# Kernel tuning notes

Hardware: AMD Instinct MI355X
Metric: run time of the kernel (lower is better)

## Reference

```python
import jax, jax.numpy as jnp
import numpy as np

B, S, HID = 16, 577, 768
H, D = 12, 64          # heads, head_dim
N_KEEP = 576           # kept channels after structured pruning


def setup_inputs() -> dict:
    key = jax.random.key(0)
    ks = jax.random.split(key, 10)
    hs = jax.random.normal(ks[0], (B, S, HID), dtype=jnp.float32)
    Wq = jax.random.normal(ks[1], (HID, N_KEEP), dtype=jnp.float32) * 0.02
    bq = jax.random.normal(ks[2], (N_KEEP,), dtype=jnp.float32) * 0.02
    Wk = jax.random.normal(ks[3], (HID, N_KEEP), dtype=jnp.float32) * 0.02
    bk = jax.random.normal(ks[4], (N_KEEP,), dtype=jnp.float32) * 0.02
    Wv = jax.random.normal(ks[5], (HID, N_KEEP), dtype=jnp.float32) * 0.02
    bv = jax.random.normal(ks[6], (N_KEEP,), dtype=jnp.float32) * 0.02
    # positions of nonzero entries of the boolean padding masks (unique, sorted)
    q_idx = jnp.sort(jax.random.permutation(ks[7], HID)[:N_KEEP]).astype(jnp.int32)
    k_idx = jnp.sort(jax.random.permutation(ks[8], HID)[:N_KEEP]).astype(jnp.int32)
    v_idx = jnp.sort(jax.random.permutation(ks[9], HID)[:N_KEEP]).astype(jnp.int32)
    return {"hidden_states": hs, "Wq": Wq, "bq": bq, "Wk": Wk, "bk": bk,
            "Wv": Wv, "bv": bv, "q_idx": q_idx, "k_idx": k_idx, "v_idx": v_idx}


def _pad_and_split_heads(x, idx):
    # scatter pruned channels [B,S,N_KEEP] back into full layout [B,S,HID],
    # then split into heads -> [B,H,S,D]
    padded = jnp.zeros((B, S, HID), dtype=x.dtype).at[:, :, idx].set(x)
    return padded.reshape(B, S, H, D).transpose(0, 2, 1, 3)


def reference(hidden_states, Wq, bq, Wk, bk, Wv, bv, q_idx, k_idx, v_idx):
    q = hidden_states @ Wq + bq            # [B,S,N_KEEP]
    k = hidden_states @ Wk + bk
    v = hidden_states @ Wv + bv
    ql = _pad_and_split_heads(q, q_idx)     # [B,H,S,D]
    kl = _pad_and_split_heads(k, k_idx)
    vl = _pad_and_split_heads(v, v_idx)
    scale = 1.0 / np.float32(np.sqrt(D))
    scores = jnp.einsum('bhqd,bhkd->bhqk', ql, kl) * scale  # [B,H,S,S]
    probs = jax.nn.softmax(scores, axis=-1)
    ctx = jnp.einsum('bhqk,bhkd->bhqd', probs, vl)          # [B,H,S,D]
    ctx = ctx.transpose(0, 2, 1, 3).reshape(B, S, HID)       # [B,S,HID]
    return ctx[:, :, v_idx]                                  # gather kept channels
```

## Files before the change

### kernel.cpp

```cpp
#include <hip/hip_runtime.h>
#include <hip/hip_bf16.h>
#include <cstdint>
#include <cstddef>

#define B_     16
#define S_     577
#define SP_    584
#define HID_   768
#define H_     12
#define D_     64
#define NKEEP_ 576
#define MP_    (B_ * SP_)
#define NP4    (MP_ * HID_ / 4)

typedef __bf16 bf16;
typedef __bf16 bf16x8 __attribute__((ext_vector_type(8)));
typedef float  f32x4  __attribute__((ext_vector_type(4)));

__device__ __forceinline__ void gload16(const bf16* g, bf16* l) {
    __builtin_amdgcn_global_load_lds(
        (const __attribute__((address_space(1))) unsigned int*)g,
        (__attribute__((address_space(3))) unsigned int*)l, 16, 0, 0);
}

__device__ __forceinline__ float fexp2(float x) {
#if __has_builtin(__builtin_amdgcn_exp2f)
    return __builtin_amdgcn_exp2f(x);
#else
    return exp2f(x);
#endif
}

#define WAITBAR(N) asm volatile("s_waitcnt vmcnt(" #N ") lgkmcnt(0)\n\ts_barrier" ::: "memory")

__global__ __launch_bounds__(256) void k_prep(const float* __restrict__ hs,
                                              const float* __restrict__ Wq,
                                              const float* __restrict__ Wk,
                                              const float* __restrict__ Wv,
                                              const float* __restrict__ bq,
                                              const float* __restrict__ bk,
                                              const float* __restrict__ bv,
                                              const int* __restrict__ qi,
                                              const int* __restrict__ ki,
                                              const int* __restrict__ vi,
                                              bf16* __restrict__ hs_bf,
                                              bf16* __restrict__ Wp_t,
                                              int* __restrict__ inv,
                                              float* __restrict__ bias_p) {
    __shared__ float tile[64][33];
    const int bid = blockIdx.x, t = threadIdx.x;
    if (bid < 54) {
        const int p = bid / 18;
        const int j0 = (bid % 18) * 32;
        const float* W  = (p == 0) ? Wq : (p == 1) ? Wk : Wv;
        const int* idx  = (p == 0) ? qi : (p == 1) ? ki : vi;
        bf16* dst = Wp_t + (size_t)p * HID_ * HID_;
        const int lj = t & 31, lk = t >> 5;
        const int sj = t >> 3, ke = (t & 7) * 8;
        const int c = idx[j0 + sj];
        for (int kt = 0; kt < HID_; kt += 64) {
            __syncthreads();
#pragma unroll
            for (int i = 0; i < 8; ++i)
                tile[lk + i * 8][lj] = W[(size_t)(kt + lk + i * 8) * NKEEP_ + j0 + lj];
            __syncthreads();
            union { bf16 h[8]; bf16x8 v; } o;
#pragma unroll
            for (int i = 0; i < 8; ++i) o.h[i] = (bf16)tile[ke + i][sj];
            *reinterpret_cast<bf16x8*>(dst + (size_t)c * HID_ + kt + ke) = o.v;
        }
    } else if (bid == 54) {
        for (int i = t; i < 3 * HID_; i += 256) { inv[i] = -1; bias_p[i] = 0.0f; }
        __syncthreads();
        for (int i = t; i < 3 * NKEEP_; i += 256) {
            const int p = i / NKEEP_, j = i % NKEEP_;
            const int* src = (p == 0) ? qi : (p == 1) ? ki : vi;
            const float* bb = (p == 0) ? bq : (p == 1) ? bk : bv;
            const int c = src[j];
            inv[p * HID_ + c] = j;
            bias_p[p * HID_ + c] = bb[j];
        }
    } else {
        const int i = (bid - 55) * 256 + t;
        if (i < NP4) {
            const int row = i / 192;
            const int col = i - row * 192;
            const int b = row / SP_;
            const int s = row - b * SP_;
            uint2 ov = {0u, 0u};
            if (s < S_) {
                float4 v = reinterpret_cast<const float4*>(hs)[((size_t)(b * S_ + s)) * 192 + col];
                union { bf16 h[4]; uint2 u; } o;
                o.h[0] = (bf16)v.x; o.h[1] = (bf16)v.y;
                o.h[2] = (bf16)v.z; o.h[3] = (bf16)v.w;
                ov = o.u;
            }
            reinterpret_cast<uint2*>(hs_bf)[(size_t)row * 192 + col] = ov;
        }
    }
}

#define BM 128
#define BN 256
#define BK 32
#define BUFE 12288

__global__ __launch_bounds__(256, 2) void k_gemm(const bf16* __restrict__ X,
                                                 const bf16* __restrict__ Wp_t,
                                                 const float* __restrict__ bias_p,
                                                 bf16* __restrict__ Qo, bf16* __restrict__ Ko,
                                                 bf16* __restrict__ Vt) {
    __shared__ bf16 smem[3 * BUFE];

    const int xcd = blockIdx.x & 7, pos = blockIdx.x >> 3;
    const int L = xcd * 82 + (xcd > 0 ? 1 : 0) + pos;
    const int m0 = (L / 9) * BM;
    const int np = L % 9;
    const int n0 = (np % 3) * BN;
    const int p  = np / 3;

    const bf16* Wbase = Wp_t + (size_t)p * HID_ * HID_;
    const float osc = (p == 0) ? 0.125f * 1.44269504f : 1.0f;

    const int t = threadIdx.x;
    const int wid = t >> 6, lane = t & 63;
    const int wr = wid >> 1, wc = wid & 1;
    const int lrow = lane & 15, g = lane >> 4, lk = (lane >> 4) * 8;
    const int srow = lane >> 2, scol = (lane & 3) * 8;

    const bf16* Xs = X + (size_t)m0 * HID_;
    const bf16* Ws = Wbase + (size_t)n0 * HID_;

    f32x4 acc[4][8] = {};

#define STAGE(buf, kk)                                                          \
    {                                                                           \
        _Pragma("unroll")                                                       \
        for (int i_ = 0; i_ < 2; ++i_) {                                        \
            const int c_ = wid * 2 + i_;                                        \
            gload16(Xs + (size_t)(c_ * 16 + srow) * HID_ + (kk) + scol,         \
                    smem + (buf) * BUFE + c_ * 512);                            \
        }                                                                       \
        _Pragma("unroll")                                                       \
        for (int i_ = 0; i_ < 4; ++i_) {                                        \
            const int c_ = wid * 4 + i_;                                        \
            gload16(Ws + (size_t)(c_ * 16 + srow) * HID_ + (kk) + scol,         \
                    smem + (buf) * BUFE + 4096 + c_ * 512);                     \
        }                                                                       \
    }

#define COMPUTE(buf)                                                            \
    {                                                                           \
        const bf16* As_ = smem + (buf) * BUFE;                                  \
        const bf16* Bs_ = As_ + 4096;                                           \
        bf16x8 af[4], bfr[8];                                                   \
        _Pragma("unroll")                                                       \
        for (int m = 0; m < 4; ++m)                                             \
            af[m] = *reinterpret_cast<const bf16x8*>(                           \
                &As_[(wr * 64 + m * 16 + lrow) * BK + lk]);                     \
        _Pragma("unroll")                                                       \
        for (int n = 0; n < 8; ++n)                                             \
            bfr[n] = *reinterpret_cast<const bf16x8*>(                          \
                &Bs_[(wc * 128 + n * 16 + lrow) * BK + lk]);                    \
        _Pragma("unroll")                                                       \
        for (int m = 0; m < 4; ++m)                                             \
            _Pragma("unroll")                                                   \
            for (int n = 0; n < 8; ++n)                                         \
                acc[m][n] = __builtin_amdgcn_mfma_f32_16x16x32_bf16(            \
                    af[m], bfr[n], acc[m][n], 0, 0, 0);                         \
    }

    STAGE(0, 0)
    STAGE(1, BK)
    WAITBAR(6);

    int kk_next = 2 * BK;
    for (int u = 0; u < 7; ++u) {
#pragma unroll
        for (int j = 0; j < 3; ++j) {
            STAGE((j + 2) % 3, kk_next)
            COMPUTE(j)
            WAITBAR(6);
            kk_next += BK;
        }
    }
    STAGE(2, 23 * BK)
    COMPUTE(0)
    WAITBAR(6);
    COMPUTE(1)
    WAITBAR(0);
    COMPUTE(2)
#undef STAGE
#undef COMPUTE

    float bias_n[8];
#pragma unroll
    for (int n = 0; n < 8; ++n)
        bias_n[n] = bias_p[p * HID_ + n0 + wc * 128 + n * 16 + lrow];

    const int rowl = t >> 2, cq = t & 3;
#pragma unroll
    for (int half = 0; half < 2; ++half) {
        __syncthreads();
        if (wr == half) {
#pragma unroll
            for (int n = 0; n < 8; ++n)
#pragma unroll
                for (int m = 0; m < 4; ++m)
#pragma unroll
                    for (int r = 0; r < 4; ++r)
                        smem[(m * 16 + g * 4 + r) * 260 + wc * 128 + n * 16 + lrow] =
                            (bf16)((acc[m][n][r] + bias_n[n]) * osc);
        }
        __syncthreads();
        const int grow0 = m0 + half * 64;
        if (p < 2) {
            bf16* Obase = (p == 0) ? Qo : Ko;
            const int grow = grow0 + rowl;
            const int b = grow / SP_, s = grow - b * SP_;
            const size_t rbase = ((size_t)(b * H_ + 0) * SP_) * D_;
#pragma unroll
            for (int i = 0; i < 4; ++i) {
                const int c0 = i * 64 + cq * 8;
                (void)rbase; (void)c0;
            }
#pragma unroll
            for (int i = 0; i < 8; ++i) {
                const int c0 = i * 32 + cq * 8;
                bf16x8 v = *reinterpret_cast<const bf16x8*>(&smem[rowl * 260 + c0]);
                const int c = n0 + c0, h = c >> 6, d = c & 63;
                *reinterpret_cast<bf16x8*>(
                    &Obase[(((size_t)(b * H_ + h) * SP_) + s) * D_ + d]) = v;
            }
        } else {
            const int crow = n0 + t;
            bf16* vrow = Vt + (size_t)crow * MP_;
#pragma unroll
            for (int rg = 0; rg < 8; ++rg) {
                union { bf16 h8[8]; bf16x8 v; } pk;
#pragma unroll
                for (int i = 0; i < 8; ++i)
                    pk.h8[i] = smem[(rg * 8 + i) * 260 + t];
                *reinterpret_cast<bf16x8*>(&vrow[grow0 + rg * 8]) = pk.v;
            }
        }
    }
}

#define KB2  64
#define VLD2 72
#define KVSZ (KB2 * VLD2)

__global__ __launch_bounds__(512, 4) void k_attn(const bf16* __restrict__ Q,
                                                 const bf16* __restrict__ K,
                                                 const bf16* __restrict__ Vt,
                                                 const int* __restrict__ inv,
                                                 float* __restrict__ out) {
    __shared__ bf16 Ksm[2][KVSZ];
    __shared__ bf16 Vsm[2][KVSZ];

    const int bid = blockIdx.x;
    const int bh = bid % (B_ * H_);
    const int q0 = (bid / (B_ * H_)) * 128;
    const int t = threadIdx.x, wid = t >> 6, lane = t & 63;
    const int lcol = lane & 15, g = lane >> 4;
    const int b = bh / H_, h = bh % H_;

    const bf16* Qb = Q + (size_t)bh * SP_ * D_;
    const bf16* Kb = K + (size_t)bh * SP_ * D_;

    const int qrow = q0 + wid * 16 + lcol;
    bf16x8 qf0 = *reinterpret_cast<const bf16x8*>(Qb + (size_t)qrow * D_ + g * 8);
    bf16x8 qf1 = *reinterpret_cast<const bf16x8*>(Qb + (size_t)qrow * D_ + 32 + g * 8);

    const int key_t = t >> 3;
    const int a_t = t & 7;
    const int ch_t = a_t * 8;
    const bf16* Vrow = Vt + (size_t)(h * D_ + key_t) * MP_ + (size_t)b * SP_;

    float lrun = 0.f;
    f32x4 oT[4] = {};

    bf16x8 kreg = *reinterpret_cast<const bf16x8*>(Kb + (size_t)key_t * D_ + ch_t);
    bf16x8 vreg = *reinterpret_cast<const bf16x8*>(Vrow + ch_t);

    int cur = 0;
    for (int k0 = 0; k0 < S_; k0 += KB2) {
        *reinterpret_cast<bf16x8*>(&Ksm[cur][key_t * VLD2 + ch_t]) = kreg;
        *reinterpret_cast<bf16x8*>(&Vsm[cur][key_t * VLD2 + ch_t]) = vreg;
        __syncthreads();

        if (k0 + KB2 < S_) {
            kreg = *reinterpret_cast<const bf16x8*>(Kb + (size_t)(k0 + KB2 + key_t) * D_ + ch_t);
            vreg = *reinterpret_cast<const bf16x8*>(Vrow + k0 + KB2 + ch_t);
        }

        f32x4 sv[4];
        __builtin_amdgcn_s_setprio(1);
#pragma unroll
        for (int ks = 0; ks < 4; ++ks) {
            const bf16* kr = &Ksm[cur][(ks * 16 + lcol) * VLD2];
            bf16x8 kf0 = *reinterpret_cast<const bf16x8*>(kr + g * 8);
            bf16x8 kf1 = *reinterpret_cast<const bf16x8*>(kr + 32 + g * 8);
            f32x4 z = {};
            z = __builtin_amdgcn_mfma_f32_16x16x32_bf16(kf0, qf0, z, 0, 0, 0);
            z = __builtin_amdgcn_mfma_f32_16x16x32_bf16(kf1, qf1, z, 0, 0, 0);
            sv[ks] = z;
        }
        __builtin_amdgcn_s_setprio(0);
        if (k0 + KB2 > S_) {
#pragma unroll
            for (int ks = 0; ks < 4; ++ks)
#pragma unroll
                for (int r = 0; r < 4; ++r)
                    if (k0 + ks * 16 + g * 4 + r >= S_) sv[ks][r] = -INFINITY;
        }

        union { bf16 h[16]; bf16x8 v[2]; } pu;
        float rs = 0.f;
#pragma unroll
        for (int ks = 0; ks < 4; ++ks)
#pragma unroll
            for (int r = 0; r < 4; ++r) {
                float pv = fexp2(sv[ks][r]);
                rs += pv;
                pu.h[ks * 4 + r] = (bf16)pv;
            }
        lrun += rs;

        __builtin_amdgcn_s_setprio(1);
#pragma unroll
        for (int kh = 0; kh < 2; ++kh) {
#pragma unroll
            for (int tt = 0; tt < 4; ++tt) {
                const int d = tt * 16 + lcol;
                const bf16* vr = &Vsm[cur][d * VLD2 + kh * 32 + 4 * g];
                union { uint2 u[2]; bf16x8 v8; } vf;
                vf.u[0] = *reinterpret_cast<const uint2*>(vr);
                vf.u[1] = *reinterpret_cast<const uint2*>(vr + 16);
                oT[tt] = __builtin_amdgcn_mfma_f32_16x16x32_bf16(vf.v8, pu.v[kh], oT[tt], 0, 0, 0);
            }
        }
        __builtin_amdgcn_s_setprio(0);
        cur ^= 1;
    }

    lrun += __shfl_xor(lrun, 16);
    lrun += __shfl_xor(lrun, 32);

    if (qrow < S_) {
        const int* invv = inv + 2 * HID_;
        float invl = 1.0f / lrun;
        float* orow = out + ((size_t)b * S_ + qrow) * NKEEP_;
#pragma unroll
        for (int tt = 0; tt < 4; ++tt)
#pragma unroll
            for (int r = 0; r < 4; ++r) {
                int d = tt * 16 + g * 4 + r;
                int j = invv[h * D_ + d];
                if (j >= 0) orow[j] = oT[tt][r] * invl;
            }
    }
}

extern "C" void kernel_launch(void* const* d_in, const int* in_sizes, int n_in,
                              void* d_out, int out_size, void* d_ws, size_t ws_size,
                              hipStream_t stream) {
    const float* hs = (const float*)d_in[0];
    const float* Wq = (const float*)d_in[1];
    const float* bq = (const float*)d_in[2];
    const float* Wk = (const float*)d_in[3];
    const float* bk = (const float*)d_in[4];
    const float* Wv = (const float*)d_in[5];
    const float* bv = (const float*)d_in[6];
    const int* qi = (const int*)d_in[7];
    const int* ki = (const int*)d_in[8];
    const int* vi = (const int*)d_in[9];
    float* out = (float*)d_out;

    char* ws = (char*)d_ws;
    size_t off = 0;
    const size_t PAD = 8192;
    bf16* hs_bf = (bf16*)(ws + off); off += (size_t)MP_ * HID_ * 2 + PAD;
    bf16* Wp_t  = (bf16*)(ws + off); off += (size_t)3 * HID_ * HID_ * 2;
    float* bias_p = (float*)(ws + off); off += 3 * HID_ * 4;
    int* inv = (int*)(ws + off); off += 3 * HID_ * 4;
    bf16* Qw = (bf16*)(ws + off); off += (size_t)B_ * H_ * SP_ * D_ * 2 + PAD;
    bf16* Kw = (bf16*)(ws + off); off += (size_t)B_ * H_ * SP_ * D_ * 2 + PAD;
    bf16* Vt = (bf16*)(ws + off); off += (size_t)HID_ * MP_ * 2 + PAD;

    hipMemsetAsync(Wp_t, 0, (size_t)3 * HID_ * HID_ * 2, stream);
    const int nprep = 55 + (NP4 + 255) / 256;
    k_prep<<<nprep, 256, 0, stream>>>(hs, Wq, Wk, Wv, bq, bk, bv, qi, ki, vi,
                                      hs_bf, Wp_t, inv, bias_p);
    k_gemm<<<657, 256, 0, stream>>>(hs_bf, Wp_t, bias_p, Qw, Kw, Vt);
    k_attn<<<5 * B_ * H_, 512, 0, stream>>>(Qw, Kw, Vt, inv, out);
}
```

Measured before the change: 109.6 us.

## Replace triple-buffered GEMM pipeline with single-buffer loop; peel attention tail block

The QKV projection GEMM drops its three-stage async global-to-LDS pipeline with fine-grained waitcnt barriers. In its place is a simple single-buffer loop that syncs before and after each K-slice load, which shrinks LDS to allow more residency. The attention kernel peels the final partial key block out of the main loop, so the steady-state iterations lose the bounds check and masking branches. The GEMM change gives up load/compute overlap and will likely expose memory latency.

```diff
diff --git a/kernel.cpp b/kernel.cpp
--- a/kernel.cpp
+++ b/kernel.cpp
@@ -30,8 +30,6 @@
     return exp2f(x);
 #endif
 }
-
-#define WAITBAR(N) asm volatile("s_waitcnt vmcnt(" #N ") lgkmcnt(0)\n\ts_barrier" ::: "memory")
 
 __global__ __launch_bounds__(256) void k_prep(const float* __restrict__ hs,
                                               const float* __restrict__ Wq,
@@ -103,14 +101,14 @@
 #define BM 128
 #define BN 256
 #define BK 32
-#define BUFE 12288
+#define SMEME 16640
 
 __global__ __launch_bounds__(256, 2) void k_gemm(const bf16* __restrict__ X,
                                                  const bf16* __restrict__ Wp_t,
                                                  const float* __restrict__ bias_p,
                                                  bf16* __restrict__ Qo, bf16* __restrict__ Ko,
                                                  bf16* __restrict__ Vt) {
-    __shared__ bf16 smem[3 * BUFE];
+    __shared__ bf16 smem[SMEME];
 
     const int xcd = blockIdx.x & 7, pos = blockIdx.x >> 3;
     const int L = xcd * 82 + (xcd > 0 ? 1 : 0) + pos;
@@ -133,65 +131,35 @@
 
     f32x4 acc[4][8] = {};
 
-#define STAGE(buf, kk)                                                          \
-    {                                                                           \
-        _Pragma("unroll")                                                       \
-        for (int i_ = 0; i_ < 2; ++i_) {                                        \
-            const int c_ = wid * 2 + i_;                                        \
-            gload16(Xs + (size_t)(c_ * 16 + srow) * HID_ + (kk) + scol,         \
-                    smem + (buf) * BUFE + c_ * 512);                            \
-        }                                                                       \
-        _Pragma("unroll")                                                       \
-        for (int i_ = 0; i_ < 4; ++i_) {                                        \
-            const int c_ = wid * 4 + i_;                                        \
-            gload16(Ws + (size_t)(c_ * 16 + srow) * HID_ + (kk) + scol,         \
-                    smem + (buf) * BUFE + 4096 + c_ * 512);                     \
-        }                                                                       \
-    }
-
-#define COMPUTE(buf)                                                            \
-    {                                                                           \
-        const bf16* As_ = smem + (buf) * BUFE;                                  \
-        const bf16* Bs_ = As_ + 4096;                                           \
-        bf16x8 af[4], bfr[8];                                                   \
-        _Pragma("unroll")                                                       \
-        for (int m = 0; m < 4; ++m)                                             \
-            af[m] = *reinterpret_cast<const bf16x8*>(                           \
-                &As_[(wr * 64 + m * 16 + lrow) * BK + lk]);                     \
-        _Pragma("unroll")                                                       \
-        for (int n = 0; n < 8; ++n)                                             \
-            bfr[n] = *reinterpret_cast<const bf16x8*>(                          \
-                &Bs_[(wc * 128 + n * 16 + lrow) * BK + lk]);                    \
-        _Pragma("unroll")                                                       \
-        for (int m = 0; m < 4; ++m)                                             \
-            _Pragma("unroll")                                                   \
-            for (int n = 0; n < 8; ++n)                                         \
-                acc[m][n] = __builtin_amdgcn_mfma_f32_16x16x32_bf16(            \
-                    af[m], bfr[n], acc[m][n], 0, 0, 0);                         \
-    }
-
-    STAGE(0, 0)
-    STAGE(1, BK)
-    WAITBAR(6);
-
-    int kk_next = 2 * BK;
-    for (int u = 0; u < 7; ++u) {
-#pragma unroll
-        for (int j = 0; j < 3; ++j) {
-            STAGE((j + 2) % 3, kk_next)
-            COMPUTE(j)
-            WAITBAR(6);
-            kk_next += BK;
-        }
-    }
-    STAGE(2, 23 * BK)
-    COMPUTE(0)
-    WAITBAR(6);
-    COMPUTE(1)
-    WAITBAR(0);
-    COMPUTE(2)
-#undef STAGE
-#undef COMPUTE
+    for (int kk = 0; kk < HID_; kk += BK) {
+        __syncthreads();
+#pragma unroll
+        for (int i_ = 0; i_ < 2; ++i_) {
+            const int c_ = wid * 2 + i_;
+            gload16(Xs + (size_t)(c_ * 16 + srow) * HID_ + kk + scol, smem + c_ * 512);
+        }
+#pragma unroll
+        for (int i_ = 0; i_ < 4; ++i_) {
+            const int c_ = wid * 4 + i_;
+            gload16(Ws + (size_t)(c_ * 16 + srow) * HID_ + kk + scol, smem + 4096 + c_ * 512);
+        }
+        __syncthreads();
+
+        const bf16* As_ = smem;
+        const bf16* Bs_ = smem + 4096;
+        bf16x8 af[4], bfr[8];
+#pragma unroll
+        for (int m = 0; m < 4; ++m)
+            af[m] = *reinterpret_cast<const bf16x8*>(&As_[(wr * 64 + m * 16 + lrow) * BK + lk]);
+#pragma unroll
+        for (int n = 0; n < 8; ++n)
+            bfr[n] = *reinterpret_cast<const bf16x8*>(&Bs_[(wc * 128 + n * 16 + lrow) * BK + lk]);
+#pragma unroll
+        for (int m = 0; m < 4; ++m)
+#pragma unroll
+            for (int n = 0; n < 8; ++n)
+                acc[m][n] = __builtin_amdgcn_mfma_f32_16x16x32_bf16(af[m], bfr[n], acc[m][n], 0, 0, 0);
+    }
 
     float bias_n[8];
 #pragma unroll
@@ -218,12 +186,6 @@
             bf16* Obase = (p == 0) ? Qo : Ko;
             const int grow = grow0 + rowl;
             const int b = grow / SP_, s = grow - b * SP_;
-            const size_t rbase = ((size_t)(b * H_ + 0) * SP_) * D_;
-#pragma unroll
-            for (int i = 0; i < 4; ++i) {
-                const int c0 = i * 64 + cq * 8;
-                (void)rbase; (void)c0;
-            }
 #pragma unroll
             for (int i = 0; i < 8; ++i) {
                 const int c0 = i * 32 + cq * 8;
@@ -285,15 +247,13 @@
     bf16x8 vreg = *reinterpret_cast<const bf16x8*>(Vrow + ch_t);
 
     int cur = 0;
-    for (int k0 = 0; k0 < S_; k0 += KB2) {
+    for (int k0 = 0; k0 < 576; k0 += KB2) {
         *reinterpret_cast<bf16x8*>(&Ksm[cur][key_t * VLD2 + ch_t]) = kreg;
         *reinterpret_cast<bf16x8*>(&Vsm[cur][key_t * VLD2 + ch_t]) = vreg;
         __syncthreads();
 
-        if (k0 + KB2 < S_) {
-            kreg = *reinterpret_cast<const bf16x8*>(Kb + (size_t)(k0 + KB2 + key_t) * D_ + ch_t);
-            vreg = *reinterpret_cast<const bf16x8*>(Vrow + k0 + KB2 + ch_t);
-        }
+        kreg = *reinterpret_cast<const bf16x8*>(Kb + (size_t)(k0 + KB2 + key_t) * D_ + ch_t);
+        vreg = *reinterpret_cast<const bf16x8*>(Vrow + k0 + KB2 + ch_t);
 
         f32x4 sv[4];
         __builtin_amdgcn_s_setprio(1);
@@ -308,13 +268,6 @@
             sv[ks] = z;
         }
         __builtin_amdgcn_s_setprio(0);
-        if (k0 + KB2 > S_) {
-#pragma unroll
-            for (int ks = 0; ks < 4; ++ks)
-#pragma unroll
-                for (int r = 0; r < 4; ++r)
-                    if (k0 + ks * 16 + g * 4 + r >= S_) sv[ks][r] = -INFINITY;
-        }
 
         union { bf16 h[16]; bf16x8 v[2]; } pu;
         float rs = 0.f;
@@ -343,6 +296,54 @@
         }
         __builtin_amdgcn_s_setprio(0);
         cur ^= 1;
+    }
+
+    {
+        *reinterpret_cast<bf16x8*>(&Ksm[cur][key_t * VLD2 + ch_t]) = kreg;
+        *reinterpret_cast<bf16x8*>(&Vsm[cur][key_t * VLD2 + ch_t]) = vreg;
+        __syncthreads();
+
+        f32x4 sv[4];
+#pragma unroll
+        for (int ks = 0; ks < 4; ++ks) {
+            const bf16* kr = &Ksm[cur][(ks * 16 + lcol) * VLD2];
+            bf16x8 kf0 = *reinterpret_cast<const bf16x8*>(kr + g * 8);
+            bf16x8 kf1 = *reinterpret_cast<const bf16x8*>(kr + 32 + g * 8);
+            f32x4 z = {};
+            z = __builtin_amdgcn_mfma_f32_16x16x32_bf16(kf0, qf0, z, 0, 0, 0);
+            z = __builtin_amdgcn_mfma_f32_16x16x32_bf16(kf1, qf1, z, 0, 0, 0);
+            sv[ks] = z;
+        }
+#pragma unroll
+        for (int ks = 0; ks < 4; ++ks)
+#pragma unroll
+            for (int r = 0; r < 4; ++r)
+                if (576 + ks * 16 + g * 4 + r >= S_) sv[ks][r] = -INFINITY;
+
+        union { bf16 h[16]; bf16x8 v[2]; } pu;
+        float rs = 0.f;
+#pragma unroll
+        for (int ks = 0; ks < 4; ++ks)
+#pragma unroll
+            for (int r = 0; r < 4; ++r) {
+                float pv = fexp2(sv[ks][r]);
+                rs += pv;
+                pu.h[ks * 4 + r] = (bf16)pv;
+            }
+        lrun += rs;
+
+#pragma unroll
+        for (int kh = 0; kh < 2; ++kh) {
+#pragma unroll
+            for (int tt = 0; tt < 4; ++tt) {
+                const int d = tt * 16 + lcol;
+                const bf16* vr = &Vsm[cur][d * VLD2 + kh * 32 + 4 * g];
+                union { uint2 u[2]; bf16x8 v8; } vf;
+                vf.u[0] = *reinterpret_cast<const uint2*>(vr);
+                vf.u[1] = *reinterpret_cast<const uint2*>(vr + 16);
+                oT[tt] = __builtin_amdgcn_mfma_f32_16x16x32_bf16(vf.v8, pu.v[kh], oT[tt], 0, 0, 0);
+            }
+        }
     }
 
     lrun += __shfl_xor(lrun, 16);
```

Result: slower. 122.5 us (+11.7%).

## Peel final key into scalar tail and use 160-query blocks

Applied to the files above, without the earlier changes.

The attention kernel now runs 9 full 64-key tiles over the first 576 keys. The single leftover key (index 576) is handled after the loop with a scalar dot product and a rank-1 update of the accumulators, which removes the mostly-masked tenth tile and its -inf masking. Blocks grow to 640 threads (10 waves) covering 160 queries each, so 4 query blocks per head replace 5 and the padded query work shrinks. This adds per-thread guards on the cooperative loads, extra LDS for the last K/V row, and fewer, larger blocks.

```diff
diff --git a/kernel.cpp b/kernel.cpp
--- a/kernel.cpp
+++ b/kernel.cpp
@@ -218,12 +218,6 @@
             bf16* Obase = (p == 0) ? Qo : Ko;
             const int grow = grow0 + rowl;
             const int b = grow / SP_, s = grow - b * SP_;
-            const size_t rbase = ((size_t)(b * H_ + 0) * SP_) * D_;
-#pragma unroll
-            for (int i = 0; i < 4; ++i) {
-                const int c0 = i * 64 + cq * 8;
-                (void)rbase; (void)c0;
-            }
 #pragma unroll
             for (int i = 0; i < 8; ++i) {
                 const int c0 = i * 32 + cq * 8;
@@ -251,17 +245,19 @@
 #define VLD2 72
 #define KVSZ (KB2 * VLD2)
 
-__global__ __launch_bounds__(512, 4) void k_attn(const bf16* __restrict__ Q,
+__global__ __launch_bounds__(640, 7) void k_attn(const bf16* __restrict__ Q,
                                                  const bf16* __restrict__ K,
                                                  const bf16* __restrict__ Vt,
                                                  const int* __restrict__ inv,
                                                  float* __restrict__ out) {
     __shared__ bf16 Ksm[2][KVSZ];
     __shared__ bf16 Vsm[2][KVSZ];
+    __shared__ bf16 Klast[64];
+    __shared__ bf16 Vlast[64];
 
     const int bid = blockIdx.x;
     const int bh = bid % (B_ * H_);
-    const int q0 = (bid / (B_ * H_)) * 128;
+    const int q0 = (bid / (B_ * H_)) * 160;
     const int t = threadIdx.x, wid = t >> 6, lane = t & 63;
     const int lcol = lane & 15, g = lane >> 4;
     const int b = bh / H_, h = bh % H_;
@@ -273,24 +269,33 @@
     bf16x8 qf0 = *reinterpret_cast<const bf16x8*>(Qb + (size_t)qrow * D_ + g * 8);
     bf16x8 qf1 = *reinterpret_cast<const bf16x8*>(Qb + (size_t)qrow * D_ + 32 + g * 8);
 
-    const int key_t = t >> 3;
-    const int a_t = t & 7;
-    const int ch_t = a_t * 8;
+    const int key_t = (t >> 3) & 63;
+    const int ch_t = (t & 7) * 8;
     const bf16* Vrow = Vt + (size_t)(h * D_ + key_t) * MP_ + (size_t)b * SP_;
 
     float lrun = 0.f;
     f32x4 oT[4] = {};
 
-    bf16x8 kreg = *reinterpret_cast<const bf16x8*>(Kb + (size_t)key_t * D_ + ch_t);
-    bf16x8 vreg = *reinterpret_cast<const bf16x8*>(Vrow + ch_t);
+    bf16x8 kreg = {}, vreg = {};
+    if (t < 512) {
+        kreg = *reinterpret_cast<const bf16x8*>(Kb + (size_t)key_t * D_ + ch_t);
+        vreg = *reinterpret_cast<const bf16x8*>(Vrow + ch_t);
+    }
+    if (t < 8)
+        *reinterpret_cast<bf16x8*>(Klast + t * 8) =
+            *reinterpret_cast<const bf16x8*>(Kb + (size_t)576 * D_ + t * 8);
+    else if (t >= 64 && t < 128)
+        Vlast[t - 64] = Vt[(size_t)(h * D_ + (t - 64)) * MP_ + (size_t)b * SP_ + 576];
 
     int cur = 0;
-    for (int k0 = 0; k0 < S_; k0 += KB2) {
-        *reinterpret_cast<bf16x8*>(&Ksm[cur][key_t * VLD2 + ch_t]) = kreg;
-        *reinterpret_cast<bf16x8*>(&Vsm[cur][key_t * VLD2 + ch_t]) = vreg;
+    for (int k0 = 0; k0 < 576; k0 += KB2) {
+        if (t < 512) {
+            *reinterpret_cast<bf16x8*>(&Ksm[cur][key_t * VLD2 + ch_t]) = kreg;
+            *reinterpret_cast<bf16x8*>(&Vsm[cur][key_t * VLD2 + ch_t]) = vreg;
+        }
         __syncthreads();
 
-        if (k0 + KB2 < S_) {
+        if (t < 512) {
             kreg = *reinterpret_cast<const bf16x8*>(Kb + (size_t)(k0 + KB2 + key_t) * D_ + ch_t);
             vreg = *reinterpret_cast<const bf16x8*>(Vrow + k0 + KB2 + ch_t);
         }
@@ -308,13 +313,6 @@
             sv[ks] = z;
         }
         __builtin_amdgcn_s_setprio(0);
-        if (k0 + KB2 > S_) {
-#pragma unroll
-            for (int ks = 0; ks < 4; ++ks)
-#pragma unroll
-                for (int r = 0; r < 4; ++r)
-                    if (k0 + ks * 16 + g * 4 + r >= S_) sv[ks][r] = -INFINITY;
-        }
 
         union { bf16 h[16]; bf16x8 v[2]; } pu;
         float rs = 0.f;
@@ -343,6 +341,24 @@
         }
         __builtin_amdgcn_s_setprio(0);
         cur ^= 1;
+    }
+
+    {
+        bf16x8 kl0 = *reinterpret_cast<const bf16x8*>(Klast + g * 8);
+        bf16x8 kl1 = *reinterpret_cast<const bf16x8*>(Klast + 32 + g * 8);
+        float part = 0.f;
+#pragma unroll
+        for (int i = 0; i < 8; ++i)
+            part += (float)qf0[i] * (float)kl0[i] + (float)qf1[i] * (float)kl1[i];
+        part += __shfl_xor(part, 16);
+        part += __shfl_xor(part, 32);
+        float p5 = fexp2(part);
+        if (g == 0) lrun += p5;
+#pragma unroll
+        for (int tt = 0; tt < 4; ++tt)
+#pragma unroll
+            for (int r = 0; r < 4; ++r)
+                oT[tt][r] += p5 * (float)Vlast[tt * 16 + g * 4 + r];
     }
 
     lrun += __shfl_xor(lrun, 16);
@@ -394,5 +410,5 @@
     k_prep<<<nprep, 256, 0, stream>>>(hs, Wq, Wk, Wv, bq, bk, bv, qi, ki, vi,
                                       hs_bf, Wp_t, inv, bias_p);
     k_gemm<<<657, 256, 0, stream>>>(hs_bf, Wp_t, bias_p, Qw, Kw, Vt);
-    k_attn<<<5 * B_ * H_, 512, 0, stream>>>(Qw, Kw, Vt, inv, out);
-}
+    k_attn<<<4 * B_ * H_, 640, 0, stream>>>(Qw, Kw, Vt, inv, out);
+}
```

New measurement: 198.5 us. 81.0% more time.
